# Kernel tuning notes

Measured on AMD Instinct MI355X. Metric: run time of the kernel, lower is better.

Reference implementation:

```python
import jax, jax.numpy as jnp
import numpy as np

B, L, D, Q, H = 16, 2048, 1024, 1024, 256
NEG_NUM = -10000.0


def setup_inputs() -> dict:
    key = jax.random.key(0)
    ks = jax.random.split(key, 8)
    ctx = jax.random.normal(ks[0], (B, L, D), dtype=jnp.float32)
    query = jax.random.normal(ks[1], (B, Q), dtype=jnp.float32)
    mask = jax.random.randint(ks[2], (B, L), 0, 2, dtype=jnp.int32)
    # lin_in2proj: Linear(D+Q, H)
    lim1 = 1.0 / np.sqrt(D + Q)
    W1 = jax.random.uniform(ks[3], (H, D + Q), jnp.float32, -lim1, lim1)
    b1 = jax.random.uniform(ks[4], (H,), jnp.float32, -lim1, lim1)
    # lin_proj2score: weight_norm(Linear(H, 1)), dim=0 -> g scalar per row
    lim2 = 1.0 / np.sqrt(H)
    v = jax.random.uniform(ks[5], (1, H), jnp.float32, -lim2, lim2)
    g = jnp.linalg.norm(v).reshape(1, 1)  # weight_norm init: g = ||v||
    b2 = jax.random.uniform(ks[6], (1,), jnp.float32, -lim2, lim2)
    return {"ctx": ctx, "query": query, "mask": mask,
            "W1": W1, "b1": b1, "v": v, "g": g, "b2": b2}


def reference(ctx, query, mask, W1, b1, v, g, b2):
    d = ctx.shape[-1]
    # concat([ctx, query_expanded]) @ W1^T == ctx @ W1c^T + query @ W1q^T
    Wc, Wq = W1[:, :d], W1[:, d:]
    hid = jnp.tanh(jnp.einsum('bld,hd->blh', ctx, Wc)
                   + jnp.einsum('bq,hq->bh', query, Wq)[:, None, :]
                   + b1)                                 # (B, L, H)
    w2 = (g * v / jnp.linalg.norm(v))[0]                 # weight-normed row (H,)
    score = jnp.einsum('blh,h->bl', hid, w2) + b2[0]     # (B, L)
    score = jnp.where(mask == 1, NEG_NUM, score)
    p_ctx = jax.nn.softmax(score, axis=-1)               # (B, L)
    expected_ctx = jnp.einsum('bl,bld->bd', p_ctx, ctx)  # (B, D)
    return expected_ctx, p_ctx
```

## Files before the change

kernel.cpp:

```cpp
#include <hip/hip_runtime.h>
#include <hip/hip_bf16.h>

#define BB 16
#define LCTX 2048
#define DDIM 1024
#define QDIM 1024
#define HDIM 256

typedef __attribute__((ext_vector_type(8))) short short8;
typedef __attribute__((ext_vector_type(4))) short short4v;
typedef __attribute__((ext_vector_type(4))) float f32x4;

__device__ inline unsigned short f2bf(float x) {
    unsigned int u = __float_as_uint(x);
    unsigned int r = (u + 0x7fffu + ((u >> 16) & 1u)) >> 16;
    return (unsigned short)r;
}

__global__ __launch_bounds__(256) void k_prep(const float* __restrict__ query,
                                              const float* __restrict__ W1,
                                              const float* __restrict__ b1,
                                              const float* __restrict__ v,
                                              const float* __restrict__ g,
                                              float* __restrict__ qproj,
                                              unsigned short* __restrict__ Wc_sw,
                                              float* __restrict__ w2) {
    int bid = blockIdx.x;
    if (bid < 1024) {
        int b = bid >> 6;
        int hq = bid & 63;
        int wid = threadIdx.x >> 6, lane = threadIdx.x & 63;
        int h = hq * 4 + wid;
        const float* q = query + b * QDIM;
        const float* w = W1 + (size_t)h * (DDIM + QDIM) + DDIM;
        float s = 0.f;
        #pragma unroll 4
        for (int k = lane; k < QDIM; k += 64) s += q[k] * w[k];
        #pragma unroll
        for (int o = 32; o; o >>= 1) s += __shfl_down(s, o);
        if (lane == 0) qproj[b * HDIM + h] = s + b1[h];
    } else if (bid < 1280) {
        int h = bid - 1024;
        const float* src = W1 + (size_t)h * (DDIM + QDIM);
        int hx = h & 7;
        for (int d = threadIdx.x; d < DDIM; d += 256) {
            int kt = d >> 6;
            int s  = (d >> 3) & 7;
            int dl = d & 7;
            int dp = (kt << 6) + ((s ^ hx) << 3) + dl;
            Wc_sw[h * DDIM + dp] = f2bf(src[d]);
        }
    } else {
        __shared__ float red[256];
        float vv = (threadIdx.x < HDIM) ? v[threadIdx.x] : 0.f;
        red[threadIdx.x] = vv * vv;
        __syncthreads();
        for (int o = 128; o; o >>= 1) {
            if (threadIdx.x < o) red[threadIdx.x] += red[threadIdx.x + o];
            __syncthreads();
        }
        float nrm = sqrtf(red[0]);
        if (threadIdx.x < HDIM) w2[threadIdx.x] = g[0] * vv / nrm;
    }
}

__global__ __launch_bounds__(256, 3) void k_score(const float* __restrict__ ctx,
                                                  const unsigned short* __restrict__ Wc_sw,
                                                  const float* __restrict__ qproj,
                                                  const float* __restrict__ w2,
                                                  const float* __restrict__ b2p,
                                                  const int* __restrict__ mask,
                                                  float* __restrict__ e_ws,
                                                  float* __restrict__ esum_ws,
                                                  float* __restrict__ part) {
    __shared__ unsigned short At[64 * 64];
    __shared__ unsigned short Wt[256 * 64];
    int tid = threadIdx.x;
    int wid = tid >> 6, lane = tid & 63;
    int hl = lane & 15, lhi = lane >> 4;
    int bid = blockIdx.x;
    int row0 = bid * 64;
    int b = row0 >> 11;

    float qp[4], wv[4];
    #pragma unroll
    for (int ht = 0; ht < 4; ht++) {
        int h = wid * 64 + ht * 16 + hl;
        qp[ht] = qproj[b * HDIM + h];
        wv[ht] = w2[h];
    }

    f32x4 acc[4][4];
    #pragma unroll
    for (int mt = 0; mt < 4; mt++)
        #pragma unroll
        for (int ht = 0; ht < 4; ht++)
            acc[mt][ht] = (f32x4){0.f, 0.f, 0.f, 0.f};

    int srow_base = wid * 16 + (lane >> 4);
    int scol = (lane & 15) * 4;
    int chunk = (lane & 15) >> 1;
    int half8 = (lane & 1) * 4;

    for (int kt = 0; kt < 16; kt++) {
        #pragma unroll
        for (int i = 0; i < 8; i++) {
            int n = i * 256 + tid;
            const unsigned short* gsrc = Wc_sw + (size_t)(n >> 3) * DDIM + kt * 64 + (n & 7) * 8;
            __builtin_amdgcn_global_load_lds(
                (const __attribute__((address_space(1))) unsigned int*)gsrc,
                (__attribute__((address_space(3))) unsigned int*)(Wt + (i * 256 + (tid & ~63)) * 8),
                16, 0, 0);
        }
        #pragma unroll
        for (int i = 0; i < 4; i++) {
            int lrow = srow_base + i * 4;
            const float* cp = ctx + (size_t)(row0 + lrow) * DDIM + kt * 64 + scol;
            float4 cv = *(const float4*)cp;
            short4v hv = { (short)f2bf(cv.x), (short)f2bf(cv.y),
                           (short)f2bf(cv.z), (short)f2bf(cv.w) };
            *(short4v*)(At + lrow * 64 + ((chunk ^ (lrow & 7)) << 3) + half8) = hv;
        }
        __syncthreads();

        #pragma unroll
        for (int ks = 0; ks < 2; ks++) {
            int s = ks * 4 + lhi;
            short8 af[4], bfr[4];
            #pragma unroll
            for (int mt = 0; mt < 4; mt++) {
                int m = mt * 16 + hl;
                af[mt] = *(const short8*)(At + m * 64 + ((s ^ (m & 7)) << 3));
            }
            #pragma unroll
            for (int ht = 0; ht < 4; ht++) {
                int h = wid * 64 + ht * 16 + hl;
                bfr[ht] = *(const short8*)(Wt + h * 64 + ((s ^ (h & 7)) << 3));
            }
            #pragma unroll
            for (int mt = 0; mt < 4; mt++)
                #pragma unroll
                for (int ht = 0; ht < 4; ht++)
                    acc[mt][ht] = __builtin_amdgcn_mfma_f32_16x16x32_bf16(af[mt], bfr[ht], acc[mt][ht], 0, 0, 0);
        }
        __syncthreads();
    }

    float* sb  = (float*)At;
    float* sbe = sb + 256;
    #pragma unroll
    for (int mt = 0; mt < 4; mt++) {
        #pragma unroll
        for (int r = 0; r < 4; r++) {
            float partial = 0.f;
            #pragma unroll
            for (int ht = 0; ht < 4; ht++) {
                float x = acc[mt][ht][r] + qp[ht];
                x = fminf(fmaxf(x, -15.f), 15.f);
                float e2 = __expf(2.f * x);
                partial += (e2 - 1.f) / (e2 + 1.f) * wv[ht];
            }
            #pragma unroll
            for (int o = 1; o < 16; o <<= 1) partial += __shfl_xor(partial, o);
            if (hl == 0) sb[wid * 64 + mt * 16 + lhi * 4 + r] = partial;
        }
    }
    __syncthreads();

    if (tid < 64) {
        float s = sb[tid] + sb[64 + tid] + sb[128 + tid] + sb[192 + tid] + b2p[0];
        int grow = row0 + tid;
        float e = (mask[b * 2048 + (grow & 2047)] == 1) ? 0.f : __expf(s);
        e_ws[grow] = e;
        sbe[tid] = e;
        float tot = e;
        #pragma unroll
        for (int o = 32; o; o >>= 1) tot += __shfl_down(tot, o);
        if (tid == 0) esum_ws[bid] = tot;
    }
    __syncthreads();

    {
        int d0 = tid * 4;
        const float* cb = ctx + (size_t)row0 * DDIM + d0;
        float4 a = {0.f, 0.f, 0.f, 0.f};
        #pragma unroll 8
        for (int l = 0; l < 64; l++) {
            float el = sbe[l];
            float4 cc = *(const float4*)(cb + (size_t)l * DDIM);
            a.x += el * cc.x; a.y += el * cc.y; a.z += el * cc.z; a.w += el * cc.w;
        }
        *(float4*)(part + (size_t)bid * DDIM + d0) = a;
    }
}

__global__ __launch_bounds__(256) void k_norm(const float* __restrict__ e_ws,
                                              const float* __restrict__ esum_ws,
                                              const float* __restrict__ part,
                                              float* __restrict__ out_exp,
                                              float* __restrict__ out_p) {
    int b = blockIdx.x, dc = blockIdx.y;
    int tid = threadIdx.x;
    float se = 0.f;
    #pragma unroll
    for (int j = 0; j < 32; j++) se += esum_ws[b * 32 + j];
    float inv = 1.f / se;
    if (tid < 128) {
        int d = dc * 128 + tid;
        float s = 0.f;
        #pragma unroll
        for (int j = 0; j < 32; j++) s += part[(size_t)(b * 32 + j) * DDIM + d];
        out_exp[b * DDIM + d] = s * inv;
    }
    int l = dc * 256 + tid;
    out_p[b * LCTX + l] = e_ws[b * LCTX + l] * inv;
}

extern "C" void kernel_launch(void* const* d_in, const int* in_sizes, int n_in,
                              void* d_out, int out_size, void* d_ws, size_t ws_size,
                              hipStream_t stream) {
    const float* ctx   = (const float*)d_in[0];
    const float* query = (const float*)d_in[1];
    const int*   mask  = (const int*)d_in[2];
    const float* W1    = (const float*)d_in[3];
    const float* b1    = (const float*)d_in[4];
    const float* v     = (const float*)d_in[5];
    const float* g     = (const float*)d_in[6];
    const float* b2    = (const float*)d_in[7];
    float* out_exp = (float*)d_out;
    float* out_p   = (float*)d_out + 16384;

    char* ws = (char*)d_ws;
    unsigned short* Wc_sw = (unsigned short*)ws;
    float* qproj = (float*)(ws + 524288);
    float* w2    = (float*)(ws + 540672);
    float* e_ws  = (float*)(ws + 541696);
    float* esum  = (float*)(ws + 672768);
    float* part  = (float*)(ws + 674816);

    k_prep <<<dim3(1281),   256, 0, stream>>>(query, W1, b1, v, g, qproj, Wc_sw, w2);
    k_score<<<dim3(512),    256, 0, stream>>>(ctx, Wc_sw, qproj, w2, b2, mask, e_ws, esum, part);
    k_norm <<<dim3(16, 8),  256, 0, stream>>>(e_ws, esum, part, out_exp, out_p);
}
```

Before: 59.59 us.

## Double-buffer ctx tiles in registers and read weights directly from global memory

The score kernel drops the shared-memory staging of the 256x64 weight tile. The weights are now stored in a k-major bf16 layout so each wave can load its MFMA B fragments straight from global memory (L2). The ctx A tile is prefetched into registers one k-step ahead and written to a double-buffered LDS tile, so there is one barrier pair per step. It also adds setprio around the MFMAs and lowers launch bounds to 2 waves per SIMD. The aim is to overlap global loads with compute and cut LDS traffic, at the cost of more global/L2 reads of the weights and more registers.

New measurement: 76.07 us. 27.7% more time.

```diff
diff --git a/kernel.cpp b/kernel.cpp
--- a/kernel.cpp
+++ b/kernel.cpp
@@ -23,7 +23,7 @@
                                               const float* __restrict__ v,
                                               const float* __restrict__ g,
                                               float* __restrict__ qproj,
-                                              unsigned short* __restrict__ Wc_sw,
+                                              unsigned short* __restrict__ Wc_kmaj,
                                               float* __restrict__ w2) {
     int bid = blockIdx.x;
     if (bid < 1024) {
@@ -42,13 +42,10 @@
     } else if (bid < 1280) {
         int h = bid - 1024;
         const float* src = W1 + (size_t)h * (DDIM + QDIM);
-        int hx = h & 7;
         for (int d = threadIdx.x; d < DDIM; d += 256) {
             int kt = d >> 6;
-            int s  = (d >> 3) & 7;
-            int dl = d & 7;
-            int dp = (kt << 6) + ((s ^ hx) << 3) + dl;
-            Wc_sw[h * DDIM + dp] = f2bf(src[d]);
+            int ko = d & 63;
+            Wc_kmaj[(size_t)kt * 16384 + h * 64 + ko] = f2bf(src[d]);
         }
     } else {
         __shared__ float red[256];
@@ -64,8 +61,8 @@
     }
 }
 
-__global__ __launch_bounds__(256, 3) void k_score(const float* __restrict__ ctx,
-                                                  const unsigned short* __restrict__ Wc_sw,
+__global__ __launch_bounds__(256, 2) void k_score(const float* __restrict__ ctx,
+                                                  const unsigned short* __restrict__ Wc_kmaj,
                                                   const float* __restrict__ qproj,
                                                   const float* __restrict__ w2,
                                                   const float* __restrict__ b2p,
@@ -73,8 +70,7 @@
                                                   float* __restrict__ e_ws,
                                                   float* __restrict__ esum_ws,
                                                   float* __restrict__ part) {
-    __shared__ unsigned short At[64 * 64];
-    __shared__ unsigned short Wt[256 * 64];
+    __shared__ unsigned short At[2][64 * 64];
     int tid = threadIdx.x;
     int wid = tid >> 6, lane = tid & 63;
     int hl = lane & 15, lhi = lane >> 4;
@@ -82,6 +78,89 @@
     int row0 = bid * 64;
     int b = row0 >> 11;
 
+    f32x4 acc[4][4];
+    #pragma unroll
+    for (int mt = 0; mt < 4; mt++)
+        #pragma unroll
+        for (int ht = 0; ht < 4; ht++)
+            acc[mt][ht] = (f32x4){0.f, 0.f, 0.f, 0.f};
+
+    int srow_base = wid * 16 + lhi;
+    int scol = (lane & 15) * 4;
+    int chunk = (lane & 15) >> 1;
+    int half8 = (lane & 1) * 4;
+
+    const unsigned short* bbase = Wc_kmaj + (size_t)(wid * 64 + hl) * 64 + lhi * 8;
+
+    float4 xa0, xa1, xa2, xa3, ya0, ya1, ya2, ya3;
+
+#define LOAD_A(KT, R0, R1, R2, R3) do { \
+    const float* cp_ = ctx + (size_t)(row0 + srow_base) * DDIM + (KT) * 64 + scol; \
+    R0 = *(const float4*)(cp_);                    \
+    R1 = *(const float4*)(cp_ + 4 * DDIM);         \
+    R2 = *(const float4*)(cp_ + 8 * DDIM);         \
+    R3 = *(const float4*)(cp_ + 12 * DDIM); } while (0)
+
+#define WRITE_A(BUF, R0, R1, R2, R3) do { \
+    short4v h0_ = { (short)f2bf(R0.x), (short)f2bf(R0.y), (short)f2bf(R0.z), (short)f2bf(R0.w) }; \
+    short4v h1_ = { (short)f2bf(R1.x), (short)f2bf(R1.y), (short)f2bf(R1.z), (short)f2bf(R1.w) }; \
+    short4v h2_ = { (short)f2bf(R2.x), (short)f2bf(R2.y), (short)f2bf(R2.z), (short)f2bf(R2.w) }; \
+    short4v h3_ = { (short)f2bf(R3.x), (short)f2bf(R3.y), (short)f2bf(R3.z), (short)f2bf(R3.w) }; \
+    int r0_ = srow_base;                                                     \
+    *(short4v*)(&At[BUF][(r0_     ) * 64 + ((chunk ^ ((r0_     ) & 7)) << 3) + half8]) = h0_; \
+    *(short4v*)(&At[BUF][(r0_ +  4) * 64 + ((chunk ^ ((r0_ + 4) & 7)) << 3) + half8]) = h1_; \
+    *(short4v*)(&At[BUF][(r0_ +  8) * 64 + ((chunk ^ ((r0_ + 8) & 7)) << 3) + half8]) = h2_; \
+    *(short4v*)(&At[BUF][(r0_ + 12) * 64 + ((chunk ^ ((r0_ +12) & 7)) << 3) + half8]) = h3_; } while (0)
+
+#define BODY(KT, DO_A, C0, C1, C2, C3, N0, N1, N2, N3) do { \
+    if (DO_A) { LOAD_A((KT) + 1, N0, N1, N2, N3); } \
+    WRITE_A((KT) & 1, C0, C1, C2, C3); \
+    asm volatile("s_waitcnt lgkmcnt(0)" ::: "memory"); \
+    __builtin_amdgcn_s_barrier(); \
+    __builtin_amdgcn_sched_barrier(0); \
+    _Pragma("unroll") \
+    for (int ks_ = 0; ks_ < 2; ks_++) { \
+        int s_ = ks_ * 4 + lhi; \
+        short8 af_[4], bf_[4]; \
+        _Pragma("unroll") \
+        for (int mt_ = 0; mt_ < 4; mt_++) { \
+            int m_ = mt_ * 16 + hl; \
+            af_[mt_] = *(const short8*)(&At[(KT) & 1][m_ * 64 + ((s_ ^ (m_ & 7)) << 3)]); \
+        } \
+        _Pragma("unroll") \
+        for (int ht_ = 0; ht_ < 4; ht_++) \
+            bf_[ht_] = *(const short8*)(bbase + (size_t)(KT) * 16384 + ht_ * 1024 + ks_ * 32); \
+        __builtin_amdgcn_s_setprio(1); \
+        _Pragma("unroll") \
+        for (int mt_ = 0; mt_ < 4; mt_++) \
+            _Pragma("unroll") \
+            for (int ht_ = 0; ht_ < 4; ht_++) \
+                acc[mt_][ht_] = __builtin_amdgcn_mfma_f32_16x16x32_bf16(af_[mt_], bf_[ht_], acc[mt_][ht_], 0, 0, 0); \
+        __builtin_amdgcn_s_setprio(0); \
+    } \
+    __builtin_amdgcn_s_barrier(); } while (0)
+
+    LOAD_A(0, xa0, xa1, xa2, xa3);
+
+    BODY( 0, 1,  xa0, xa1, xa2, xa3,  ya0, ya1, ya2, ya3);
+    BODY( 1, 1,  ya0, ya1, ya2, ya3,  xa0, xa1, xa2, xa3);
+    BODY( 2, 1,  xa0, xa1, xa2, xa3,  ya0, ya1, ya2, ya3);
+    BODY( 3, 1,  ya0, ya1, ya2, ya3,  xa0, xa1, xa2, xa3);
+    BODY( 4, 1,  xa0, xa1, xa2, xa3,  ya0, ya1, ya2, ya3);
+    BODY( 5, 1,  ya0, ya1, ya2, ya3,  xa0, xa1, xa2, xa3);
+    BODY( 6, 1,  xa0, xa1, xa2, xa3,  ya0, ya1, ya2, ya3);
+    BODY( 7, 1,  ya0, ya1, ya2, ya3,  xa0, xa1, xa2, xa3);
+    BODY( 8, 1,  xa0, xa1, xa2, xa3,  ya0, ya1, ya2, ya3);
+    BODY( 9, 1,  ya0, ya1, ya2, ya3,  xa0, xa1, xa2, xa3);
+    BODY(10, 1,  xa0, xa1, xa2, xa3,  ya0, ya1, ya2, ya3);
+    BODY(11, 1,  ya0, ya1, ya2, ya3,  xa0, xa1, xa2, xa3);
+    BODY(12, 1,  xa0, xa1, xa2, xa3,  ya0, ya1, ya2, ya3);
+    BODY(13, 1,  ya0, ya1, ya2, ya3,  xa0, xa1, xa2, xa3);
+    BODY(14, 1,  xa0, xa1, xa2, xa3,  ya0, ya1, ya2, ya3);
+    BODY(15, 0,  ya0, ya1, ya2, ya3,  xa0, xa1, xa2, xa3);
+
+    __syncthreads();
+
     float qp[4], wv[4];
     #pragma unroll
     for (int ht = 0; ht < 4; ht++) {
@@ -89,63 +168,6 @@
         qp[ht] = qproj[b * HDIM + h];
         wv[ht] = w2[h];
     }
-
-    f32x4 acc[4][4];
-    #pragma unroll
-    for (int mt = 0; mt < 4; mt++)
-        #pragma unroll
-        for (int ht = 0; ht < 4; ht++)
-            acc[mt][ht] = (f32x4){0.f, 0.f, 0.f, 0.f};
-
-    int srow_base = wid * 16 + (lane >> 4);
-    int scol = (lane & 15) * 4;
-    int chunk = (lane & 15) >> 1;
-    int half8 = (lane & 1) * 4;
-
-    for (int kt = 0; kt < 16; kt++) {
-        #pragma unroll
-        for (int i = 0; i < 8; i++) {
-            int n = i * 256 + tid;
-            const unsigned short* gsrc = Wc_sw + (size_t)(n >> 3) * DDIM + kt * 64 + (n & 7) * 8;
-            __builtin_amdgcn_global_load_lds(
-                (const __attribute__((address_space(1))) unsigned int*)gsrc,
-                (__attribute__((address_space(3))) unsigned int*)(Wt + (i * 256 + (tid & ~63)) * 8),
-                16, 0, 0);
-        }
-        #pragma unroll
-        for (int i = 0; i < 4; i++) {
-            int lrow = srow_base + i * 4;
-            const float* cp = ctx + (size_t)(row0 + lrow) * DDIM + kt * 64 + scol;
-            float4 cv = *(const float4*)cp;
-            short4v hv = { (short)f2bf(cv.x), (short)f2bf(cv.y),
-                           (short)f2bf(cv.z), (short)f2bf(cv.w) };
-            *(short4v*)(At + lrow * 64 + ((chunk ^ (lrow & 7)) << 3) + half8) = hv;
-        }
-        __syncthreads();
-
-        #pragma unroll
-        for (int ks = 0; ks < 2; ks++) {
-            int s = ks * 4 + lhi;
-            short8 af[4], bfr[4];
-            #pragma unroll
-            for (int mt = 0; mt < 4; mt++) {
-                int m = mt * 16 + hl;
-                af[mt] = *(const short8*)(At + m * 64 + ((s ^ (m & 7)) << 3));
-            }
-            #pragma unroll
-            for (int ht = 0; ht < 4; ht++) {
-                int h = wid * 64 + ht * 16 + hl;
-                bfr[ht] = *(const short8*)(Wt + h * 64 + ((s ^ (h & 7)) << 3));
-            }
-            #pragma unroll
-            for (int mt = 0; mt < 4; mt++)
-                #pragma unroll
-                for (int ht = 0; ht < 4; ht++)
-                    acc[mt][ht] = __builtin_amdgcn_mfma_f32_16x16x32_bf16(af[mt], bfr[ht], acc[mt][ht], 0, 0, 0);
-        }
-        __syncthreads();
-    }
-
     float* sb  = (float*)At;
     float* sbe = sb + 256;
     #pragma unroll
@@ -231,14 +253,14 @@
     float* out_p   = (float*)d_out + 16384;
 
     char* ws = (char*)d_ws;
-    unsigned short* Wc_sw = (unsigned short*)ws;
+    unsigned short* Wc_kmaj = (unsigned short*)ws;
     float* qproj = (float*)(ws + 524288);
     float* w2    = (float*)(ws + 540672);
     float* e_ws  = (float*)(ws + 541696);
     float* esum  = (float*)(ws + 672768);
     float* part  = (float*)(ws + 674816);
 
-    k_prep <<<dim3(1281),   256, 0, stream>>>(query, W1, b1, v, g, qproj, Wc_sw, w2);
-    k_score<<<dim3(512),    256, 0, stream>>>(ctx, Wc_sw, qproj, w2, b2, mask, e_ws, esum, part);
+    k_prep <<<dim3(1281),   256, 0, stream>>>(query, W1, b1, v, g, qproj, Wc_kmaj, w2);
+    k_score<<<dim3(512),    256, 0, stream>>>(ctx, Wc_kmaj, qproj, w2, b2, mask, e_ws, esum, part);
     k_norm <<<dim3(16, 8),  256, 0, stream>>>(e_ws, esum, part, out_exp, out_p);
 }
```
